# Optimization experiments

Hardware: AMD Instinct MI355X
Metric: run time of the kernel (lower is better)

Reference implementation:

```python
import jax, jax.numpy as jnp
import numpy as np

N_NODES = 100000
N_EDGES = 1600000
N_GRAPHS = 64
VOCAB = 50000
D = 128
EPS = 1e-5


def setup_inputs() -> dict:
    key = jax.random.key(0)
    ks = jax.random.split(key, 24)
    tokens = jax.random.randint(ks[0], (N_NODES,), 0, VOCAB)
    src = jax.random.randint(ks[1], (N_EDGES,), 0, N_NODES)
    dst = jax.random.randint(ks[2], (N_EDGES,), 0, N_NODES)
    graph_ids = jnp.sort(jax.random.randint(ks[3], (N_NODES,), 0, N_GRAPHS))
    s = 1.0 / np.sqrt(D)
    inp = {
        'tokens': tokens, 'src': src, 'dst': dst, 'graph_ids': graph_ids,
        'embed': jax.random.normal(ks[4], (VOCAB, D), jnp.float32),
        'W1': jax.random.normal(ks[5], (D, D), jnp.float32) * s,
        'b1': jnp.zeros((D,), jnp.float32),
        'g1': jnp.ones((D,), jnp.float32), 'be1': jnp.zeros((D,), jnp.float32),
        'W2': jax.random.normal(ks[6], (D, D), jnp.float32) * s,
        'b2': jnp.zeros((D,), jnp.float32),
        'g2': jnp.ones((D,), jnp.float32), 'be2': jnp.zeros((D,), jnp.float32),
        'W3': jax.random.normal(ks[7], (D, D), jnp.float32) * s,
        'b3': jnp.zeros((D,), jnp.float32),
        'g3': jnp.ones((D,), jnp.float32), 'be3': jnp.zeros((D,), jnp.float32),
        'fcW1': jax.random.normal(ks[8], (D, D // 2), jnp.float32) * s,
        'fcb1': jnp.zeros((D // 2,), jnp.float32),
        'fcW2': jax.random.normal(ks[9], (D // 2, 2), jnp.float32) * (1.0 / np.sqrt(D // 2)),
        'fcb2': jnp.zeros((2,), jnp.float32),
    }
    return inp


def _graph_conv(h, src, dst, norm_src, norm_dst, W, b):
    # DGL GraphConv, norm='both': D_out^{-1/2} -> sum-aggregate -> D_in^{-1/2} -> linear
    msg = (h * norm_src[:, None])[src]                      # [E, D]
    agg = jax.ops.segment_sum(msg, dst, num_segments=N_NODES)
    return (agg * norm_dst[:, None]) @ W + b


def _bn_relu(h, gamma, beta):
    mu = jnp.mean(h, axis=0)
    var = jnp.mean((h - mu) ** 2, axis=0)                   # biased var (torch BN)
    return jax.nn.relu((h - mu) * jax.lax.rsqrt(var + EPS) * gamma + beta)


def reference(tokens, src, dst, graph_ids, embed,
              W1, b1, g1, be1, W2, b2, g2, be2, W3, b3, g3, be3,
              fcW1, fcb1, fcW2, fcb2):
    ones_e = jnp.ones((N_EDGES,), jnp.float32)
    deg_out = jnp.maximum(jax.ops.segment_sum(ones_e, src, num_segments=N_NODES), 1.0)
    deg_in = jnp.maximum(jax.ops.segment_sum(ones_e, dst, num_segments=N_NODES), 1.0)
    norm_src = jax.lax.rsqrt(deg_out)
    norm_dst = jax.lax.rsqrt(deg_in)

    h = embed[tokens]                                        # [N, D]
    h = _bn_relu(_graph_conv(h, src, dst, norm_src, norm_dst, W1, b1), g1, be1)
    h = _bn_relu(_graph_conv(h, src, dst, norm_src, norm_dst, W2, b2), g2, be2)
    h = _bn_relu(_graph_conv(h, src, dst, norm_src, norm_dst, W3, b3), g3, be3)

    # dgl.mean_nodes per graph
    sums = jax.ops.segment_sum(h, graph_ids, num_segments=N_GRAPHS)  # [G, D]
    cnts = jnp.maximum(jax.ops.segment_sum(jnp.ones((N_NODES,), jnp.float32), graph_ids, num_segments=N_GRAPHS), 1.0)
    hg = sums / cnts[:, None]

    hg = jax.nn.relu(hg @ fcW1 + fcb1)                       # dropout = identity (eval)
    return hg @ fcW2 + fcb2                                  # [G, 2]
```

## Files before the change

### kernel.cpp

```cpp
#include <hip/hip_runtime.h>

#define N_NODES 100000
#define N_EDGES 1600000
#define N_GRAPHS 64
#define DIM 128
#define BN_EPS 1e-5f
#define EPAD 2000000

#define NB_SENT 977
#define NB_WPREP 192
#define NB_HIST 391
#define NB_ZERO 40
#define NBUCK 782
#define NG (NBUCK * NB_HIST)
#define NB_SCANG2 2389
#define BUCK_RESERVE 388

#define AT_STRIDE 136

typedef unsigned short ushort_t;
typedef unsigned char uchar_t;
typedef unsigned int uint_t;
typedef __attribute__((ext_vector_type(8))) short bf16x8;
typedef __attribute__((ext_vector_type(4))) float f32x4;

__device__ __forceinline__ float bfl(uint_t u) {
    union { uint_t i; float f; } v; v.i = u << 16; return v.f;
}
__device__ __forceinline__ float bfh(uint_t u) {
    union { uint_t i; float f; } v; v.i = u & 0xffff0000u; return v.f;
}
__device__ __forceinline__ ushort_t f2bf(float f) {
    union { float f; uint_t i; } v; v.f = f;
    uint_t x = v.i;
    return (ushort_t)((x + 0x7fffu + ((x >> 16) & 1u)) >> 16);
}
__device__ __forceinline__ uint_t pack2(float lo, float hi) {
    return ((uint_t)f2bf(hi) << 16) | (uint_t)f2bf(lo);
}

__global__ void k_front(const int* __restrict__ src, const int* __restrict__ dst,
                        ushort_t* __restrict__ bufA, int* __restrict__ esrc,
                        const float* __restrict__ w1, const float* __restrict__ w2,
                        const float* __restrict__ w3, ushort_t* __restrict__ wbt,
                        int* __restrict__ GG, int* __restrict__ zp, int zwords) {
    __shared__ int hh[NBUCK];
    __shared__ int hh2[NBUCK];
    int b = blockIdx.x;
    int t = threadIdx.x;
    if (b < NB_SENT) {
        int i0 = (b * 256 + t) * 8;
        int4 sv = make_int4(N_NODES, N_NODES, N_NODES, N_NODES);
        if (i0 + 8 <= EPAD) {
            *(int4*)(esrc + i0) = sv;
            *(int4*)(esrc + i0 + 4) = sv;
        } else {
            for (int i = i0; i < EPAD; ++i) esrc[i] = N_NODES;
        }
        if (b == 0 && t < 64)
            ((uint_t*)(bufA + (size_t)N_NODES * DIM))[t] = 0u;
        return;
    }
    b -= NB_SENT;
    if (b < NB_WPREP) {
        int i = b * 256 + t;
        int l = i >> 14;
        int idx = i & (DIM * DIM - 1);
        int n = idx >> 7, k = idx & (DIM - 1);
        const float* wsrc = (l == 0) ? w1 : (l == 1) ? w2 : w3;
        wbt[i] = f2bf(wsrc[k * DIM + n]);
        return;
    }
    b -= NB_WPREP;
    if (b < NB_HIST) {
        for (int k = t; k < NBUCK; k += 256) { hh[k] = 0; hh2[k] = 0; }
        __syncthreads();
        int e0 = b * 4096;
        int e1 = min(e0 + 4096, N_EDGES);
        for (int i = e0 + t; i < e1; i += 256) {
            atomicAdd(&hh[dst[i] >> 7], 1);
            atomicAdd(&hh2[src[i] >> 7], 1);
        }
        __syncthreads();
        for (int k = t; k < NBUCK; k += 256) {
            GG[k * NB_HIST + b] = hh[k];
            GG[NG + k * NB_HIST + b] = hh2[k];
        }
        return;
    }
    b -= NB_HIST;
    {
        int i = b * 256 + t;
        if (i < zwords) zp[i] = 0;
    }
}

__global__ void k_scanA(const int* __restrict__ GG, int* __restrict__ Gs,
                        int* __restrict__ partials) {
    __shared__ int s[256];
    int t = threadIdx.x;
    int i = blockIdx.x * 256 + t;
    int v = (i < 2 * NG) ? GG[i] : 0;
    s[t] = v;
    __syncthreads();
    for (int off = 1; off < 256; off <<= 1) {
        int add = (t >= off) ? s[t - off] : 0;
        __syncthreads();
        s[t] += add;
        __syncthreads();
    }
    if (i < 2 * NG) Gs[i + 1] = s[t];
    if (t == 255) partials[blockIdx.x] = s[t];
}

__global__ void k_scanB(const int* __restrict__ partials, int* __restrict__ Gs) {
    __shared__ int s[256];
    int t = threadIdx.x;
    int p = 0;
    for (int j = t; j < (int)blockIdx.x; j += 256) p += partials[j];
    s[t] = p;
    __syncthreads();
    for (int off = 128; off > 0; off >>= 1) {
        if (t < off) s[t] += s[t + off];
        __syncthreads();
    }
    int prefix = s[0];
    int i = blockIdx.x * 256 + t;
    if (i < 2 * NG) Gs[i + 1] += prefix;
    if (blockIdx.x == 0 && t == 0) Gs[0] = 0;
}

__global__ void k_pass2(const int* __restrict__ src, const int* __restrict__ dst,
                        const int* __restrict__ Gs, int* __restrict__ Csrc,
                        uchar_t* __restrict__ Cdl, uchar_t* __restrict__ Cls) {
    __shared__ int cur[NBUCK];
    __shared__ int cur2[NBUCK];
    int b = blockIdx.x;
    int t = threadIdx.x;
    for (int k = t; k < NBUCK; k += 256) {
        cur[k] = Gs[k * NB_HIST + b];
        cur2[k] = Gs[NG + k * NB_HIST + b] - N_EDGES;
    }
    __syncthreads();
    int e0 = b * 4096;
    int e1 = min(e0 + 4096, N_EDGES);
    for (int i = e0 + t; i < e1; i += 256) {
        int d = dst[i];
        int s = src[i];
        int slot = atomicAdd(&cur[d >> 7], 1);
        Csrc[slot] = s;
        Cdl[slot] = (uchar_t)(d & 127);
        int slot2 = atomicAdd(&cur2[s >> 7], 1);
        Cls[slot2] = (uchar_t)(s & 127);
    }
}

__global__ void k_fine(const int* __restrict__ Csrc, const uchar_t* __restrict__ Cdl,
                       const uchar_t* __restrict__ Cls, const int* __restrict__ Gs,
                       int* __restrict__ esrc, int* __restrict__ rowptr,
                       int* __restrict__ pdeg, float* __restrict__ ns,
                       float* __restrict__ nd) {
    __shared__ int hcnt[128];
    __shared__ int hstart[128];
    int b = blockIdx.x;
    int t = threadIdx.x;
    if (b < NBUCK) {
        int k = b;
        int node0 = k * 128;
        int nn = min(128, N_NODES - node0);
        int S = Gs[k * NB_HIST];
        int E = Gs[(k + 1) * NB_HIST];
        if (t < 128) hcnt[t] = 0;
        __syncthreads();
        for (int i = S + t; i < E; i += 256) atomicAdd(&hcnt[Cdl[i]], 1);
        __syncthreads();
        if (t == 0) {
            int acc = 0;
            for (int n = 0; n < nn; ++n) {
                hstart[n] = acc;
                acc += (hcnt[n] + 3) & ~3;
            }
        }
        __syncthreads();
        int base = (k * BUCK_RESERVE + S + 3) & ~3;
        if (t < nn) {
            int node = node0 + t;
            rowptr[node] = base + hstart[t];
            pdeg[node] = (hcnt[t] + 3) & ~3;
            nd[node] = rsqrtf(fmaxf((float)hcnt[t], 1.0f));
        }
        __syncthreads();
        for (int i = S + t; i < E; i += 256) {
            int slot = atomicAdd(&hstart[Cdl[i]], 1);
            esrc[base + slot] = Csrc[i];
        }
    } else {
        int k = b - NBUCK;
        int node0 = k * 128;
        int nn = min(128, N_NODES - node0);
        int S = Gs[NG + k * NB_HIST] - N_EDGES;
        int E = Gs[NG + (k + 1) * NB_HIST] - N_EDGES;
        if (t < 128) hcnt[t] = 0;
        __syncthreads();
        for (int i = S + t; i < E; i += 256) atomicAdd(&hcnt[Cls[i]], 1);
        __syncthreads();
        if (t < nn)
            ns[node0 + t] = rsqrtf(fmaxf((float)hcnt[t], 1.0f));
        if (k == 0 && t == 0) ns[N_NODES] = 0.f;
    }
}

__global__ void k_embed_ps(const int* __restrict__ tokens, const float* __restrict__ embed,
                           const float* __restrict__ ns, ushort_t* __restrict__ bufA) {
    int gid = blockIdx.x * 256 + threadIdx.x;
    int node = gid >> 4, sub = gid & 15;
    float s = ns[node];
    const float* ep = embed + (size_t)tokens[node] * DIM + sub * 8;
    float4 a = *(const float4*)ep;
    float4 c = *(const float4*)(ep + 4);
    uint4 o;
    o.x = pack2(a.x * s, a.y * s);
    o.y = pack2(a.z * s, a.w * s);
    o.z = pack2(c.x * s, c.y * s);
    o.w = pack2(c.z * s, c.w * s);
    *(uint4*)(bufA + (size_t)node * DIM + sub * 8) = o;
}

__global__ void k_prescale(const ushort_t* __restrict__ yin, const float* __restrict__ ns,
                           const float* __restrict__ bnsum, const float* __restrict__ bnsq,
                           const float* __restrict__ g, const float* __restrict__ be,
                           ushort_t* __restrict__ xout) {
    __shared__ float sa[DIM], sc[DIM];
    int t = threadIdx.x;
    if (t < DIM) {
        float mu = bnsum[t] * (1.0f / N_NODES);
        float var = bnsq[t] * (1.0f / N_NODES) - mu * mu;
        float rstd = rsqrtf(var + BN_EPS);
        float a = g[t] * rstd;
        sa[t] = a;
        sc[t] = be[t] - mu * a;
    }
    __syncthreads();
    int gid = blockIdx.x * 256 + t;
    int node = gid >> 4, sub = gid & 15;
    float s = ns[node];
    uint4 u = *(const uint4*)(yin + (size_t)node * DIM + sub * 8);
    float v[8] = {bfl(u.x), bfh(u.x), bfl(u.y), bfh(u.y),
                  bfl(u.z), bfh(u.z), bfl(u.w), bfh(u.w)};
    const float* a = sa + sub * 8;
    const float* c = sc + sub * 8;
#pragma unroll
    for (int i = 0; i < 8; ++i) v[i] = fmaxf(fmaf(v[i], a[i], c[i]), 0.f) * s;
    uint4 o;
    o.x = pack2(v[0], v[1]); o.y = pack2(v[2], v[3]);
    o.z = pack2(v[4], v[5]); o.w = pack2(v[6], v[7]);
    *(uint4*)(xout + (size_t)node * DIM + sub * 8) = o;
}

__global__ __launch_bounds__(256) void k_agggemm(const ushort_t* __restrict__ hs,
        const int* __restrict__ rowptr, const int* __restrict__ pdeg,
        const int* __restrict__ esrc, const float* __restrict__ nd,
        const ushort_t* __restrict__ wbt, const float* __restrict__ bias,
        ushort_t* __restrict__ y,
        float* __restrict__ bnsum, float* __restrict__ bnsq) {
    __shared__ ushort_t at[64 * AT_STRIDE];
    __shared__ float csum[DIM], csq[DIM];
    int tid = threadIdx.x;
    int wave = tid >> 6;
    int lane = tid & 63;
    if (tid < DIM) { csum[tid] = 0.f; csq[tid] = 0.f; }
    __syncthreads();

    int bnode = blockIdx.x * 64 + wave * 16;
    int off = lane * 2;

    int rpv = 0, pdv = 0;
    if (lane < 16) {
        int nnode = bnode + lane;
        if (nnode < N_NODES) { rpv = rowptr[nnode]; pdv = pdeg[nnode]; }
    }

#define LD2(s) (*(const uint_t*)(hs + (size_t)(s) * DIM + off))
#define ACC8(I0, I1, X0, Y0, X1, Y1)                                           \
    {                                                                          \
        uint_t u0 = LD2(I0.x), u1 = LD2(I0.y), u2 = LD2(I0.z), u3 = LD2(I0.w); \
        uint_t u4 = LD2(I1.x), u5 = LD2(I1.y), u6 = LD2(I1.z), u7 = LD2(I1.w); \
        X0 += bfl(u0); Y0 += bfh(u0); X1 += bfl(u1); Y1 += bfh(u1);            \
        X0 += bfl(u2); Y0 += bfh(u2); X1 += bfl(u3); Y1 += bfh(u3);            \
        X0 += bfl(u4); Y0 += bfh(u4); X1 += bfl(u5); Y1 += bfh(u5);            \
        X0 += bfl(u6); Y0 += bfh(u6); X1 += bfl(u7); Y1 += bfh(u7);            \
    }
#define ACC4(I0, X0, Y0, X1, Y1)                                               \
    {                                                                          \
        uint_t u0 = LD2(I0.x), u1 = LD2(I0.y), u2 = LD2(I0.z), u3 = LD2(I0.w); \
        X0 += bfl(u0); Y0 += bfh(u0); X1 += bfl(u1); Y1 += bfh(u1);            \
        X0 += bfl(u2); Y0 += bfh(u2); X1 += bfl(u3); Y1 += bfh(u3);            \
    }

    for (int i = 0; i < 16; i += 2) {
        int nodeA = bnode + i;
        int nodeB = bnode + i + 1;
        int eA = __shfl(rpv, i);
        int endA = eA + __shfl(pdv, i);
        int eB = __shfl(rpv, i + 1);
        int endB = eB + __shfl(pdv, i + 1);
        float xA0 = 0.f, yA0 = 0.f, xA1 = 0.f, yA1 = 0.f;
        float xB0 = 0.f, yB0 = 0.f, xB1 = 0.f, yB1 = 0.f;
        if (eA + 8 <= endA && eB + 8 <= endB) {
            int4 cA0 = *(const int4*)(esrc + eA);
            int4 cA1 = *(const int4*)(esrc + eA + 4);
            int4 cB0 = *(const int4*)(esrc + eB);
            int4 cB1 = *(const int4*)(esrc + eB + 4);
            while (true) {
                int4 nA0 = *(const int4*)(esrc + eA + 8);
                int4 nA1 = *(const int4*)(esrc + eA + 12);
                int4 nB0 = *(const int4*)(esrc + eB + 8);
                int4 nB1 = *(const int4*)(esrc + eB + 12);
                ACC8(cA0, cA1, xA0, yA0, xA1, yA1);
                ACC8(cB0, cB1, xB0, yB0, xB1, yB1);
                eA += 8; eB += 8;
                if (!(eA + 8 <= endA && eB + 8 <= endB)) break;
                cA0 = nA0; cA1 = nA1; cB0 = nB0; cB1 = nB1;
            }
        }
        for (; eA + 8 <= endA; eA += 8) {
            int4 i0 = *(const int4*)(esrc + eA);
            int4 i1 = *(const int4*)(esrc + eA + 4);
            ACC8(i0, i1, xA0, yA0, xA1, yA1);
        }
        if (eA < endA) {
            int4 i0 = *(const int4*)(esrc + eA);
            ACC4(i0, xA0, yA0, xA1, yA1);
        }
        for (; eB + 8 <= endB; eB += 8) {
            int4 i0 = *(const int4*)(esrc + eB);
            int4 i1 = *(const int4*)(esrc + eB + 4);
            ACC8(i0, i1, xB0, yB0, xB1, yB1);
        }
        if (eB < endB) {
            int4 i0 = *(const int4*)(esrc + eB);
            ACC4(i0, xB0, yB0, xB1, yB1);
        }
        uint_t ovA = 0u, ovB = 0u;
        if (nodeA < N_NODES) {
            float n = nd[nodeA];
            ovA = pack2((xA0 + xA1) * n, (yA0 + yA1) * n);
        }
        if (nodeB < N_NODES) {
            float n = nd[nodeB];
            ovB = pack2((xB0 + xB1) * n, (yB0 + yB1) * n);
        }
        *(uint_t*)&at[(wave * 16 + i) * AT_STRIDE + off] = ovA;
        *(uint_t*)&at[(wave * 16 + i + 1) * AT_STRIDE + off] = ovB;
    }
#undef ACC8
#undef ACC4
#undef LD2

    int m16 = lane & 15;
    int quad = lane >> 4;
    f32x4 acc[8];
#pragma unroll
    for (int nb = 0; nb < 8; ++nb) acc[nb] = (f32x4)(0.f);

    const ushort_t* ap = &at[(wave * 16 + m16) * AT_STRIDE + quad * 8];
#pragma unroll
    for (int k0b = 0; k0b < 4; ++k0b) {
        bf16x8 af = *(const bf16x8*)(ap + k0b * 32);
#pragma unroll
        for (int nb = 0; nb < 8; ++nb) {
            int ncol = nb * 16 + m16;
            bf16x8 bfg = *(const bf16x8*)(wbt + (size_t)ncol * DIM + k0b * 32 + quad * 8);
            acc[nb] = __builtin_amdgcn_mfma_f32_16x16x32_bf16(af, bfg, acc[nb], 0, 0, 0);
        }
    }

#pragma unroll
    for (int nb = 0; nb < 8; ++nb) {
        int col = nb * 16 + m16;
        float bcol = bias[col];
        float ps = 0.f, pq = 0.f;
#pragma unroll
        for (int reg = 0; reg < 4; ++reg) {
            int r = bnode + quad * 4 + reg;
            if (r < N_NODES) {
                float v = acc[nb][reg] + bcol;
                ps += v; pq += v * v;
                y[(size_t)r * DIM + col] = f2bf(v);
            }
        }
        atomicAdd(&csum[col], ps);
        atomicAdd(&csq[col], pq);
    }
    __syncthreads();
    if (tid < DIM) {
        atomicAdd(&bnsum[tid], csum[tid]);
        atomicAdd(&bnsq[tid], csq[tid]);
    }
}

#define POOL_NODES 128
__global__ void k_pool(const ushort_t* __restrict__ yin, const int* __restrict__ gids,
                       const float* __restrict__ bnsum, const float* __restrict__ bnsq,
                       const float* __restrict__ g, const float* __restrict__ be,
                       float* __restrict__ pool, int* __restrict__ cnt) {
    __shared__ int h[N_GRAPHS];
    int col = threadIdx.x;
    float mu = bnsum[col] * (1.0f / N_NODES);
    float var = bnsq[col] * (1.0f / N_NODES) - mu * mu;
    float rstd = rsqrtf(var + BN_EPS);
    float a = g[col] * rstd;
    float c = be[col] - mu * a;
    if (col < N_GRAPHS) h[col] = 0;
    __syncthreads();
    int base = blockIdx.x * POOL_NODES;
    int end = min(base + POOL_NODES, N_NODES);
    for (int n = base + col; n < end; n += 128) atomicAdd(&h[gids[n]], 1);
    __syncthreads();
    if (col < N_GRAPHS && h[col]) atomicAdd(&cnt[col], h[col]);
    float acc = 0.f;
    int cur = gids[base];
    for (int n = base; n < end; ++n) {
        int gg = gids[n];
        if (gg != cur) {
            atomicAdd(&pool[(size_t)cur * DIM + col], acc);
            acc = 0.f;
            cur = gg;
        }
        uint_t u = *(const uint_t*)(yin + (size_t)n * DIM + (col & ~1));
        float v = (col & 1) ? bfh(u) : bfl(u);
        acc += fmaxf(fmaf(v, a, c), 0.f);
    }
    atomicAdd(&pool[(size_t)cur * DIM + col], acc);
}

__global__ void k_final(const float* __restrict__ pool, const int* __restrict__ cnt,
                        const float* __restrict__ fcW1, const float* __restrict__ fcb1,
                        const float* __restrict__ fcW2, const float* __restrict__ fcb2,
                        float* __restrict__ out) {
    __shared__ float hg[DIM];
    __shared__ float z[64];
    int g = blockIdx.x;
    int t = threadIdx.x;
    float cf = fmaxf((float)cnt[g], 1.0f);
    hg[t] = pool[(size_t)g * DIM + t] / cf;
    __syncthreads();
    if (t < 64) {
        float acc = fcb1[t];
        for (int k = 0; k < DIM; ++k)
            acc += hg[k] * fcW1[k * 64 + t];
        z[t] = fmaxf(acc, 0.f);
    }
    __syncthreads();
    if (t < 2) {
        float acc = fcb2[t];
        for (int k = 0; k < 64; ++k)
            acc += z[k] * fcW2[k * 2 + t];
        out[g * 2 + t] = acc;
    }
}

extern "C" void kernel_launch(void* const* d_in, const int* in_sizes, int n_in,
                              void* d_out, int out_size, void* d_ws, size_t ws_size,
                              hipStream_t stream) {
    const int* tokens = (const int*)d_in[0];
    const int* src = (const int*)d_in[1];
    const int* dst = (const int*)d_in[2];
    const int* gids = (const int*)d_in[3];
    const float* embed = (const float*)d_in[4];
    const float* W1 = (const float*)d_in[5];
    const float* b1 = (const float*)d_in[6];
    const float* g1 = (const float*)d_in[7];
    const float* be1 = (const float*)d_in[8];
    const float* W2 = (const float*)d_in[9];
    const float* b2 = (const float*)d_in[10];
    const float* g2 = (const float*)d_in[11];
    const float* be2 = (const float*)d_in[12];
    const float* W3 = (const float*)d_in[13];
    const float* b3 = (const float*)d_in[14];
    const float* g3 = (const float*)d_in[15];
    const float* be3 = (const float*)d_in[16];
    const float* fcW1 = (const float*)d_in[17];
    const float* fcb1 = (const float*)d_in[18];
    const float* fcW2 = (const float*)d_in[19];
    const float* fcb2 = (const float*)d_in[20];
    float* out = (float*)d_out;

    char* w = (char*)d_ws;
    auto alloc = [&](size_t bytes) {
        void* p = (void*)w;
        w += (bytes + 255) & ~(size_t)255;
        return p;
    };
    ushort_t* bufH = (ushort_t*)alloc((size_t)(N_NODES + 1) * DIM * 2);
    ushort_t* bufA = (ushort_t*)alloc((size_t)(N_NODES + 1) * DIM * 2);
    ushort_t* bufY = (ushort_t*)alloc((size_t)(N_NODES + 1) * DIM * 2);
    int* esrc = (int*)alloc((size_t)EPAD * 4);
    int* rowptr = (int*)alloc((size_t)N_NODES * 4);
    int* pdeg = (int*)alloc((size_t)N_NODES * 4);
    float* ns = (float*)alloc((size_t)(N_NODES + 1) * 4);
    float* nd = (float*)alloc((size_t)N_NODES * 4);
    ushort_t* wbt = (ushort_t*)alloc(3 * DIM * DIM * 2);
    int* GG = (int*)alloc((size_t)(2 * NG) * 4);
    int* Gs = (int*)alloc((size_t)(2 * NG + 1) * 4);
    int* partials = (int*)alloc(4096 * 4);
    int* Csrc = (int*)alloc((size_t)N_EDGES * 4);
    uchar_t* Cdl = (uchar_t*)alloc((size_t)N_EDGES);
    uchar_t* Cls = (uchar_t*)alloc((size_t)N_EDGES);
    char* zstart = w;
    float* bnsum = (float*)alloc(3 * DIM * 4);
    float* bnsq = (float*)alloc(3 * DIM * 4);
    float* pool = (float*)alloc((size_t)N_GRAPHS * DIM * 4);
    int* cnt = (int*)alloc((size_t)N_GRAPHS * 4);
    int zwords = (int)((size_t)(w - zstart) / 4);

    k_front<<<NB_SENT + NB_WPREP + NB_HIST + NB_ZERO, 256, 0, stream>>>(
        src, dst, bufA, esrc, W1, W2, W3, wbt, GG, (int*)zstart, zwords);
    k_scanA<<<NB_SCANG2, 256, 0, stream>>>(GG, Gs, partials);
    k_scanB<<<NB_SCANG2, 256, 0, stream>>>(partials, Gs);
    k_pass2<<<NB_HIST, 256, 0, stream>>>(src, dst, Gs, Csrc, Cdl, Cls);
    k_fine<<<2 * NBUCK, 256, 0, stream>>>(Csrc, Cdl, Cls, Gs, esrc, rowptr, pdeg, ns, nd);

    int nb_fused = (N_NODES + 63) / 64;
    int nb_ps = 6250;

    k_embed_ps<<<nb_ps, 256, 0, stream>>>(tokens, embed, ns, bufA);
    k_agggemm<<<nb_fused, 256, 0, stream>>>(bufA, rowptr, pdeg, esrc, nd,
                                            wbt, b1, bufY, bnsum, bnsq);
    k_prescale<<<nb_ps, 256, 0, stream>>>(bufY, ns, bnsum, bnsq, g1, be1, bufA);
    k_agggemm<<<nb_fused, 256, 0, stream>>>(bufA, rowptr, pdeg, esrc, nd,
                                            wbt + (size_t)DIM * DIM, b2, bufH,
                                            bnsum + DIM, bnsq + DIM);
    k_prescale<<<nb_ps, 256, 0, stream>>>(bufH, ns, bnsum + DIM, bnsq + DIM, g2, be2, bufA);
    k_agggemm<<<nb_fused, 256, 0, stream>>>(bufA, rowptr, pdeg, esrc, nd,
                                            wbt + (size_t)2 * DIM * DIM, b3, bufY,
                                            bnsum + 2 * DIM, bnsq + 2 * DIM);

    k_pool<<<(N_NODES + POOL_NODES - 1) / POOL_NODES, DIM, 0, stream>>>(
        bufY, gids, bnsum + 2 * DIM, bnsq + 2 * DIM, g3, be3, pool, cnt);
    k_final<<<N_GRAPHS, DIM, 0, stream>>>(pool, cnt, fcW1, fcb1, fcW2, fcb2, out);
}
```

Baseline: 655.6 us.

## Pack src and dst-local into one word and fuse embedding gather into k_fine

The scatter pass now stores the source index (17 bits) and the destination's low 7 bits in a single 32-bit word instead of separate int and byte arrays, which cuts stores and loads in the bucketing passes. The embedding gather and out-degree prescale move into the out-degree half of k_fine, using the per-node norms already held in shared memory, so the separate k_embed_ps launch and its global reads of ns are removed. The cost is more work per k_fine block in that half, which may unbalance it against the in-degree blocks.

```diff
diff --git a/kernel.cpp b/kernel.cpp
--- a/kernel.cpp
+++ b/kernel.cpp
@@ -131,8 +131,8 @@
 }
 
 __global__ void k_pass2(const int* __restrict__ src, const int* __restrict__ dst,
-                        const int* __restrict__ Gs, int* __restrict__ Csrc,
-                        uchar_t* __restrict__ Cdl, uchar_t* __restrict__ Cls) {
+                        const int* __restrict__ Gs, uint_t* __restrict__ Cpk,
+                        uchar_t* __restrict__ Cls) {
     __shared__ int cur[NBUCK];
     __shared__ int cur2[NBUCK];
     int b = blockIdx.x;
@@ -148,20 +148,21 @@
         int d = dst[i];
         int s = src[i];
         int slot = atomicAdd(&cur[d >> 7], 1);
-        Csrc[slot] = s;
-        Cdl[slot] = (uchar_t)(d & 127);
+        Cpk[slot] = (uint_t)s | ((uint_t)(d & 127) << 17);
         int slot2 = atomicAdd(&cur2[s >> 7], 1);
         Cls[slot2] = (uchar_t)(s & 127);
     }
 }
 
-__global__ void k_fine(const int* __restrict__ Csrc, const uchar_t* __restrict__ Cdl,
-                       const uchar_t* __restrict__ Cls, const int* __restrict__ Gs,
+__global__ void k_fine(const uint_t* __restrict__ Cpk, const uchar_t* __restrict__ Cls,
+                       const int* __restrict__ Gs,
+                       const int* __restrict__ tokens, const float* __restrict__ embed,
                        int* __restrict__ esrc, int* __restrict__ rowptr,
                        int* __restrict__ pdeg, float* __restrict__ ns,
-                       float* __restrict__ nd) {
+                       float* __restrict__ nd, ushort_t* __restrict__ bufA) {
     __shared__ int hcnt[128];
     __shared__ int hstart[128];
+    __shared__ float lns[128];
     int b = blockIdx.x;
     int t = threadIdx.x;
     if (b < NBUCK) {
@@ -172,7 +173,7 @@
         int E = Gs[(k + 1) * NB_HIST];
         if (t < 128) hcnt[t] = 0;
         __syncthreads();
-        for (int i = S + t; i < E; i += 256) atomicAdd(&hcnt[Cdl[i]], 1);
+        for (int i = S + t; i < E; i += 256) atomicAdd(&hcnt[Cpk[i] >> 17], 1);
         __syncthreads();
         if (t == 0) {
             int acc = 0;
@@ -191,8 +192,9 @@
         }
         __syncthreads();
         for (int i = S + t; i < E; i += 256) {
-            int slot = atomicAdd(&hstart[Cdl[i]], 1);
-            esrc[base + slot] = Csrc[i];
+            uint_t pk = Cpk[i];
+            int slot = atomicAdd(&hstart[pk >> 17], 1);
+            esrc[base + slot] = (int)(pk & 0x1FFFFu);
         }
     } else {
         int k = b - NBUCK;
@@ -204,26 +206,28 @@
         __syncthreads();
         for (int i = S + t; i < E; i += 256) atomicAdd(&hcnt[Cls[i]], 1);
         __syncthreads();
-        if (t < nn)
-            ns[node0 + t] = rsqrtf(fmaxf((float)hcnt[t], 1.0f));
+        if (t < nn) {
+            float v = rsqrtf(fmaxf((float)hcnt[t], 1.0f));
+            ns[node0 + t] = v;
+            lns[t] = v;
+        }
         if (k == 0 && t == 0) ns[N_NODES] = 0.f;
-    }
-}
-
-__global__ void k_embed_ps(const int* __restrict__ tokens, const float* __restrict__ embed,
-                           const float* __restrict__ ns, ushort_t* __restrict__ bufA) {
-    int gid = blockIdx.x * 256 + threadIdx.x;
-    int node = gid >> 4, sub = gid & 15;
-    float s = ns[node];
-    const float* ep = embed + (size_t)tokens[node] * DIM + sub * 8;
-    float4 a = *(const float4*)ep;
-    float4 c = *(const float4*)(ep + 4);
-    uint4 o;
-    o.x = pack2(a.x * s, a.y * s);
-    o.y = pack2(a.z * s, a.w * s);
-    o.z = pack2(c.x * s, c.y * s);
-    o.w = pack2(c.z * s, c.w * s);
-    *(uint4*)(bufA + (size_t)node * DIM + sub * 8) = o;
+        __syncthreads();
+        for (int slot = t; slot < nn * 16; slot += 256) {
+            int nloc = slot >> 4, sub = slot & 15;
+            int node = node0 + nloc;
+            float s = lns[nloc];
+            const float* ep = embed + (size_t)tokens[node] * DIM + sub * 8;
+            float4 a = *(const float4*)ep;
+            float4 c = *(const float4*)(ep + 4);
+            uint4 o;
+            o.x = pack2(a.x * s, a.y * s);
+            o.y = pack2(a.z * s, a.w * s);
+            o.z = pack2(c.x * s, c.y * s);
+            o.w = pack2(c.z * s, c.w * s);
+            *(uint4*)(bufA + (size_t)node * DIM + sub * 8) = o;
+        }
+    }
 }
 
 __global__ void k_prescale(const ushort_t* __restrict__ yin, const float* __restrict__ ns,
@@ -504,8 +508,7 @@
     int* GG = (int*)alloc((size_t)(2 * NG) * 4);
     int* Gs = (int*)alloc((size_t)(2 * NG + 1) * 4);
     int* partials = (int*)alloc(4096 * 4);
-    int* Csrc = (int*)alloc((size_t)N_EDGES * 4);
-    uchar_t* Cdl = (uchar_t*)alloc((size_t)N_EDGES);
+    uint_t* Cpk = (uint_t*)alloc((size_t)N_EDGES * 4);
     uchar_t* Cls = (uchar_t*)alloc((size_t)N_EDGES);
     char* zstart = w;
     float* bnsum = (float*)alloc(3 * DIM * 4);
@@ -518,13 +521,13 @@
         src, dst, bufA, esrc, W1, W2, W3, wbt, GG, (int*)zstart, zwords);
     k_scanA<<<NB_SCANG2, 256, 0, stream>>>(GG, Gs, partials);
     k_scanB<<<NB_SCANG2, 256, 0, stream>>>(partials, Gs);
-    k_pass2<<<NB_HIST, 256, 0, stream>>>(src, dst, Gs, Csrc, Cdl, Cls);
-    k_fine<<<2 * NBUCK, 256, 0, stream>>>(Csrc, Cdl, Cls, Gs, esrc, rowptr, pdeg, ns, nd);
+    k_pass2<<<NB_HIST, 256, 0, stream>>>(src, dst, Gs, Cpk, Cls);
+    k_fine<<<2 * NBUCK, 256, 0, stream>>>(Cpk, Cls, Gs, tokens, embed,
+                                          esrc, rowptr, pdeg, ns, nd, bufA);
 
     int nb_fused = (N_NODES + 63) / 64;
     int nb_ps = 6250;
 
-    k_embed_ps<<<nb_ps, 256, 0, stream>>>(tokens, embed, ns, bufA);
     k_agggemm<<<nb_fused, 256, 0, stream>>>(bufA, rowptr, pdeg, esrc, nd,
                                             wbt, b1, bufY, bnsum, bnsq);
     k_prescale<<<nb_ps, 256, 0, stream>>>(bufY, ns, bnsum, bnsq, g1, be1, bufA);
```

Result: faster. 633.7 us (-3.3%).
